# Performance work log

Measured on AMD Instinct MI355X. Metric: run time of the kernel, lower is better.

The kernel has to match this reference:

```python
import jax, jax.numpy as jnp
import numpy as np

EMB = 512
HEADS = 8
HD = EMB // HEADS
DEPTH = 6
CONT = 100
CAT_DIMS = [100] * 28
CAT = len(CAT_DIMS)
HID = int(EMB * (4.0 / 3.0))  # 682, FT-Transformer ReGLU hidden
B = 128
OFFSETS = jnp.asarray(np.concatenate([[0], np.cumsum(CAT_DIMS[:-1])]).astype(np.int32))
SQRT_EMB = float(np.sqrt(EMB))  # scores are DIVIDED by emb**-0.5 in the source


def setup_inputs() -> dict:
    key = jax.random.key(0)
    ks = jax.random.split(key, 16)
    s = 0.02
    x_cat = jax.random.randint(ks[0], (B, CAT), 0, CAT_DIMS[0]).astype(jnp.float32)
    x_cont = jax.random.normal(ks[1], (B, CONT), dtype=jnp.float32)
    x = jnp.concatenate([x_cat, x_cont], axis=1)  # [B, CAT+CONT]
    return {
        "x": x,
        "tok_w": jax.random.normal(ks[2], (CONT + 1, EMB)) * s,
        "tok_b": jax.random.normal(ks[3], (CONT + CAT, EMB)) * s,
        "cat_emb": jax.random.normal(ks[4], (sum(CAT_DIMS), EMB)) * s,
        "Wqkv": jax.random.normal(ks[5], (DEPTH, EMB, 3 * EMB)) * s,
        "bqkv": jnp.zeros((DEPTH, 3 * EMB)),
        "Wout": jax.random.normal(ks[6], (DEPTH, EMB, EMB)) * s,
        "bout": jnp.zeros((DEPTH, EMB)),
        "W0": jax.random.normal(ks[7], (DEPTH, EMB, 2 * HID)) * s,
        "b0": jnp.zeros((DEPTH, 2 * HID)),
        "W1": jax.random.normal(ks[8], (DEPTH, HID, EMB)) * s,
        "b1": jnp.zeros((DEPTH, EMB)),
        "ln0_g": jnp.ones((DEPTH, EMB)),
        "ln0_b": jnp.zeros((DEPTH, EMB)),
        "ln1_g": jnp.ones((DEPTH, EMB)),
        "ln1_b": jnp.zeros((DEPTH, EMB)),
    }


def _ln(x, g, b):
    m = x.mean(-1, keepdims=True)
    v = x.var(-1, keepdims=True)
    return (x - m) / jnp.sqrt(v + 1e-5) * g + b


def _attn(x, Wqkv, bqkv, Wout, bout):
    Bn, S, _ = x.shape
    # faithful layout: reshape to (B,S,H,3*hd), move heads, chunk last dim
    qkv = (x @ Wqkv + bqkv).reshape(Bn, S, HEADS, 3 * HD).transpose(0, 2, 1, 3)
    q, k, v = jnp.split(qkv, 3, axis=-1)  # each [B,H,S,hd]
    scores = jnp.einsum("bhqd,bhkd->bhqk", q, k) * SQRT_EMB  # / (emb**-0.5)
    attn = jax.nn.softmax(jax.nn.softmax(scores, axis=-1), axis=-1)  # double softmax, as in source
    o = jnp.einsum("bhqk,bhkd->bhqd", attn, v)
    o = o.transpose(0, 2, 1, 3).reshape(Bn, S, EMB)
    return o @ Wout + bout


def _reglu(x):
    a, b = jnp.split(x, 2, axis=-1)
    return a * jax.nn.relu(b)


def _forward(x, tok_w, tok_b, cat_emb, Wqkv, bqkv, Wout, bout, W0, b0, W1, b1,
             ln0_g, ln0_b, ln1_g, ln1_b):
    # --- feature tokenizer ---
    x_cats = x[:, :CAT].astype(jnp.int32)
    x_conts = jnp.concatenate([jnp.ones((x.shape[0], 1), x.dtype), x[:, CAT:]], axis=1)  # [B, CONT+1]
    h = tok_w[None] * x_conts[:, :, None]  # [B, CONT+1, EMB]
    h = jnp.concatenate([h, cat_emb[x_cats + OFFSETS[None]]], axis=1)  # [B, S=129, EMB]
    bias = jnp.concatenate([jnp.zeros((1, EMB), h.dtype), tok_b], axis=0)
    h = h + bias[None]
    # --- transformer stack ---
    for i in range(DEPTH):
        xin = _ln(h, ln0_g[i], ln0_b[i]) if i else h  # layer 0 has no norm0
        h = h + _attn(xin, Wqkv[i], bqkv[i], Wout[i], bout[i])
        r = _ln(h, ln1_g[i], ln1_b[i])
        r = _reglu(r @ W0[i] + b0[i]) @ W1[i] + b1[i]
        h = h + r
    return h[:, 0]  # CLS token


def reference(x, tok_w, tok_b, cat_emb, Wqkv, bqkv, Wout, bout, W0, b0, W1, b1,
              ln0_g, ln0_b, ln1_g, ln1_b):
    return _forward(x, tok_w, tok_b, cat_emb, Wqkv, bqkv, Wout, bout, W0, b0, W1, b1,
                    ln0_g, ln0_b, ln1_g, ln1_b)
```

## Files before the change

kernel.cpp:

```cpp
#include <hip/hip_runtime.h>
#include <hip/hip_bf16.h>
#include <stdint.h>


typedef __hip_bfloat16 bf16_t;
typedef __attribute__((ext_vector_type(8))) __bf16 bf16x8;
typedef __attribute__((ext_vector_type(4))) float floatx4;

constexpr int M_ROWS = 16512;
constexpr float SQRT_EMB_F = 22.627416997969522f;

__device__ __forceinline__ floatx4 mfma16(bf16x8 a, bf16x8 b, floatx4 c) {
  return __builtin_amdgcn_mfma_f32_16x16x32_bf16(a, b, c, 0, 0, 0);
}

__device__ __forceinline__ size_t frag_chunk(int m, int k, int KT) {
  return ((size_t)(m >> 4) * KT + (k >> 5)) * 512 + (m & 15) * 8 + 128 * ((k >> 3) & 3);
}
__device__ __forceinline__ size_t frag_elem(int m, int k, int KT) {
  return frag_chunk(m, k, KT) + (k & 7);
}

template <int PERM>
__global__ __launch_bounds__(256) void transpose_cvt(const float* __restrict__ W,
    bf16_t* __restrict__ WT, int K, int N, int KP, int NP)
{
  __shared__ float tile[32][33];
  int k0 = blockIdx.x * 32, n0 = blockIdx.y * 32;
  const float* Wl = W + (size_t)blockIdx.z * K * N;
  bf16_t* WTl = WT + (size_t)blockIdx.z * NP * KP;
  const int KT = KP >> 5;
  #pragma unroll
  for (int r = 0; r < 32; r += 8) {
    int k = k0 + threadIdx.y + r, n = n0 + threadIdx.x;
    int srcn = PERM ? ((n & 1) ? 682 + (n >> 1) : (n >> 1)) : n;
    int valid = (k < K) && (PERM ? (n < 1364) : (n < N));
    tile[threadIdx.y + r][threadIdx.x] = valid ? Wl[(size_t)k * N + srcn] : 0.f;
  }
  __syncthreads();
  #pragma unroll
  for (int r = 0; r < 32; r += 8) {
    int n = n0 + threadIdx.y + r, k = k0 + threadIdx.x;
    if (n < NP && k < KP)
      WTl[frag_elem(n, k, KT)] = __float2bfloat16(tile[threadIdx.x][threadIdx.y + r]);
  }
}

__global__ __launch_bounds__(256) void tokenizer_kernel(const float* __restrict__ x,
    const float* __restrict__ tok_w, const float* __restrict__ tok_b,
    const float* __restrict__ cat_emb, float* __restrict__ h, bf16_t* __restrict__ ab)
{
  int row = blockIdx.x * 4 + (threadIdx.x >> 6);
  int lane = threadIdx.x & 63, e0 = lane * 8;
  int b = row / 129, t = row - b * 129;
  float v[8];
  if (t == 0) {
    #pragma unroll
    for (int u = 0; u < 8; u++) v[u] = tok_w[e0 + u];
  } else if (t <= 100) {
    float xv = x[(size_t)b * 128 + 28 + (t - 1)];
    const float* wp = tok_w + (size_t)t * 512 + e0;
    const float* bp = tok_b + (size_t)(t - 1) * 512 + e0;
    #pragma unroll
    for (int u = 0; u < 8; u++) v[u] = wp[u] * xv + bp[u];
  } else {
    int j = t - 101;
    int idx = (int)x[(size_t)b * 128 + j] + 100 * j;
    const float* cp = cat_emb + (size_t)idx * 512 + e0;
    const float* bp = tok_b + (size_t)(t - 1) * 512 + e0;
    #pragma unroll
    for (int u = 0; u < 8; u++) v[u] = cp[u] + bp[u];
  }
  float* hr = h + (size_t)row * 512 + e0;
  #pragma unroll
  for (int u = 0; u < 8; u++) hr[u] = v[u];
  bf16x8 o8;
  #pragma unroll
  for (int u = 0; u < 8; u++) o8[u] = (__bf16)__float2bfloat16(v[u]);
  *(bf16x8*)(ab + ((size_t)(row >> 4) * 16 + (lane >> 2)) * 512 + (row & 15) * 8 + 128 * (lane & 3)) = o8;
}

__global__ __launch_bounds__(256) void ln_kernel(const float* __restrict__ hin,
    bf16_t* __restrict__ out, const float* __restrict__ g, const float* __restrict__ bta)
{
  int row = blockIdx.x * 4 + (threadIdx.x >> 6);
  int lane = threadIdx.x & 63;
  const float* hr = hin + (size_t)row * 512 + lane * 8;
  float4 v0 = *(const float4*)hr;
  float4 v1 = *(const float4*)(hr + 4);
  float s = v0.x + v0.y + v0.z + v0.w + v1.x + v1.y + v1.z + v1.w;
  float q = v0.x * v0.x + v0.y * v0.y + v0.z * v0.z + v0.w * v0.w
          + v1.x * v1.x + v1.y * v1.y + v1.z * v1.z + v1.w * v1.w;
  #pragma unroll
  for (int o = 1; o < 64; o <<= 1) { s += __shfl_xor(s, o); q += __shfl_xor(q, o); }
  float mean = s * (1.f / 512.f);
  float var = q * (1.f / 512.f) - mean * mean;
  float rstd = rsqrtf(var + 1e-5f);
  float4 g0 = *(const float4*)(g + lane * 8);
  float4 g1 = *(const float4*)(g + lane * 8 + 4);
  float4 b0v = *(const float4*)(bta + lane * 8);
  float4 b1v = *(const float4*)(bta + lane * 8 + 4);
  bf16x8 o8;
  o8[0] = (__bf16)__float2bfloat16((v0.x - mean) * rstd * g0.x + b0v.x);
  o8[1] = (__bf16)__float2bfloat16((v0.y - mean) * rstd * g0.y + b0v.y);
  o8[2] = (__bf16)__float2bfloat16((v0.z - mean) * rstd * g0.z + b0v.z);
  o8[3] = (__bf16)__float2bfloat16((v0.w - mean) * rstd * g0.w + b0v.w);
  o8[4] = (__bf16)__float2bfloat16((v1.x - mean) * rstd * g1.x + b1v.x);
  o8[5] = (__bf16)__float2bfloat16((v1.y - mean) * rstd * g1.y + b1v.y);
  o8[6] = (__bf16)__float2bfloat16((v1.z - mean) * rstd * g1.z + b1v.z);
  o8[7] = (__bf16)__float2bfloat16((v1.w - mean) * rstd * g1.w + b1v.w);
  *(bf16x8*)(out + ((size_t)(row >> 4) * 16 + (lane >> 2)) * 512 + (row & 15) * 8 + 128 * (lane & 3)) = o8;
}

template <int MODE>
__global__ __launch_bounds__(256, 3) void gemm_frag(const bf16_t* __restrict__ A,
    const bf16_t* __restrict__ BT, const float* __restrict__ bias, int biasN,
    const float* __restrict__ resid, void* __restrict__ outp, int K, int N)
{
  const int total = gridDim.x * gridDim.y;
  const int lin = blockIdx.y * gridDim.x + blockIdx.x;
  const int xcd = lin & 7, kb2 = lin >> 3;
  const int qch = total >> 3, rch = total & 7;
  const int idx = xcd * qch + (xcd < rch ? xcd : rch) + kb2;
  const int bm = idx / gridDim.x;
  const int bn = idx - bm * gridDim.x;
  const int m0 = bm * 128, n0 = bn * 128;

  const int tid = threadIdx.x;
  const int w = tid >> 6, l = tid & 63, l15 = l & 15, quad = l >> 4;
  const int wm = (w >> 1) * 64, wn = (w & 1) * 64;
  const int KT = K >> 5;

  const bf16_t* pa[4];
  const bf16_t* pb[4];
  #pragma unroll
  for (int i = 0; i < 4; i++) {
    pa[i] = A  + ((size_t)(((m0 + wm) >> 4) + i) * KT) * 512 + l * 8;
    pb[i] = BT + ((size_t)(((n0 + wn) >> 4) + i) * KT) * 512 + l * 8;
  }

  bf16x8 af[2][4], bg[2][4];
  #pragma unroll
  for (int i = 0; i < 4; i++) {
    af[0][i] = *(const bf16x8*)pa[i];
    bg[0][i] = *(const bf16x8*)pb[i];
  }

  floatx4 z4 = {0.f, 0.f, 0.f, 0.f};
  floatx4 acc[4][4];
  #pragma unroll
  for (int i = 0; i < 4; i++)
    #pragma unroll
    for (int j = 0; j < 4; j++) acc[i][j] = z4;

  const int T = KT;
  for (int t = 0; t < T; t += 2) {
    if (t + 1 < T) {
      #pragma unroll
      for (int i = 0; i < 4; i++) {
        af[1][i] = *(const bf16x8*)(pa[i] + (size_t)(t + 1) * 512);
        bg[1][i] = *(const bf16x8*)(pb[i] + (size_t)(t + 1) * 512);
      }
    }
    #pragma unroll
    for (int i = 0; i < 4; i++)
      #pragma unroll
      for (int j = 0; j < 4; j++)
        acc[i][j] = mfma16(af[0][i], bg[0][j], acc[i][j]);
    if (t + 1 < T) {
      if (t + 2 < T) {
        #pragma unroll
        for (int i = 0; i < 4; i++) {
          af[0][i] = *(const bf16x8*)(pa[i] + (size_t)(t + 2) * 512);
          bg[0][i] = *(const bf16x8*)(pb[i] + (size_t)(t + 2) * 512);
        }
      }
      #pragma unroll
      for (int i = 0; i < 4; i++)
        #pragma unroll
        for (int j = 0; j < 4; j++)
          acc[i][j] = mfma16(af[1][i], bg[1][j], acc[i][j]);
    }
  }

  #pragma unroll
  for (int j = 0; j < 4; j++) {
    int col = n0 + wn + j * 16 + l15;
    float bv = 0.f;
    if (MODE == 2) {
      if (col < biasN) bv = bias[(col & 1) ? 682 + (col >> 1) : (col >> 1)];
    } else {
      if (col < biasN) bv = bias[col];
    }
    #pragma unroll
    for (int i = 0; i < 4; i++) {
      int row_b = m0 + wm + i * 16 + quad * 4;
      #pragma unroll
      for (int r = 0; r < 4; r++) {
        float v = acc[i][j][r] + bv;
        int m = row_b + r;
        if (MODE == 2) {
          float other = __shfl_xor(v, 1);
          if (!(l15 & 1)) {
            int c2 = col >> 1;
            ((bf16_t*)outp)[frag_elem(m, c2, (N >> 1) >> 5)] =
                __float2bfloat16(v * fmaxf(other, 0.f));
          }
        } else if (MODE == 1) {
          size_t idx2 = (size_t)m * N + col;
          ((float*)outp)[idx2] = v + resid[idx2];
        } else {
          ((bf16_t*)outp)[frag_elem(m, col, N >> 5)] = __float2bfloat16(v);
        }
      }
    }
  }
}

constexpr int SP = 160;
__global__ __launch_bounds__(256) void attn_kernel(const bf16_t* __restrict__ qkv,
                                                   bf16_t* __restrict__ attnout)
{
  __shared__ bf16_t vt_lds[64 * SP];
  __shared__ float sc[32 * SP];
  bf16_t* p_lds = (bf16_t*)sc;
  __bf16* vt_raw = (__bf16*)vt_lds;

  const int bh = blockIdx.x, b = bh >> 3, hh = bh & 7;
  const int tid = threadIdx.x;
  const int w = tid >> 6, l = tid & 63, l15 = l & 15, quad = l >> 4;
  const int rbase = b * 129;

  for (int i = tid; i < SP * 64 / 2; i += 256) ((unsigned int*)vt_lds)[i] = 0u;
  __syncthreads();
  for (int c = tid; c < 129 * 8; c += 256) {
    int s = c >> 3, ch = c & 7;
    bf16x8 tv = *(const bf16x8*)(qkv + frag_chunk(rbase + s, hh * 192 + 128 + ch * 8, 48));
    #pragma unroll
    for (int j = 0; j < 8; j++) vt_raw[(size_t)(ch * 8 + j) * SP + s] = tv[j];
  }
  __syncthreads();

  for (int qt = 0; qt < 5; qt++) {
    bf16x8 zq = {};
    bf16x8 aq[2][2];
    #pragma unroll
    for (int mt = 0; mt < 2; mt++) {
      int m = qt * 32 + mt * 16 + l15;
      #pragma unroll
      for (int t = 0; t < 2; t++)
        aq[mt][t] = (m < 129)
            ? *(const bf16x8*)(qkv + frag_chunk(rbase + m, hh * 192 + t * 32 + quad * 8, 48)) : zq;
    }
    for (int nt = w; nt < 10; nt += 4) {
      int krow = nt * 16 + l15;
      floatx4 a0 = {0.f, 0.f, 0.f, 0.f}, a1 = {0.f, 0.f, 0.f, 0.f};
      #pragma unroll
      for (int t = 0; t < 2; t++) {
        bf16x8 kf = (krow < 129)
            ? *(const bf16x8*)(qkv + frag_chunk(rbase + krow, hh * 192 + 64 + t * 32 + quad * 8, 48))
            : zq;
        a0 = mfma16(aq[0][t], kf, a0);
        a1 = mfma16(aq[1][t], kf, a1);
      }
      #pragma unroll
      for (int r = 0; r < 4; r++) {
        sc[(quad * 4 + r) * SP + nt * 16 + l15]      = a0[r] * SQRT_EMB_F;
        sc[(16 + quad * 4 + r) * SP + nt * 16 + l15] = a1[r] * SQRT_EMB_F;
      }
    }
    __syncthreads();

    {
      int row = tid >> 3, sub = tid & 7;
      float vv[20];
      float mx = -1e30f;
      #pragma unroll
      for (int c = 0; c < 20; c++) {
        int j = sub + c * 8;
        vv[c] = (j < 129) ? sc[row * SP + j] : -1e30f;
        mx = fmaxf(mx, vv[c]);
      }
      #pragma unroll
      for (int o = 1; o < 8; o <<= 1) mx = fmaxf(mx, __shfl_xor(mx, o, 8));
      float sum = 0.f;
      #pragma unroll
      for (int c = 0; c < 20; c++) {
        int j = sub + c * 8;
        vv[c] = (j < 129) ? __expf(vv[c] - mx) : 0.f;
        sum += vv[c];
      }
      #pragma unroll
      for (int o = 1; o < 8; o <<= 1) sum += __shfl_xor(sum, o, 8);
      float inv = 1.f / sum;
      float mx2 = 0.f;
      #pragma unroll
      for (int c = 0; c < 20; c++) { vv[c] *= inv; mx2 = fmaxf(mx2, vv[c]); }
      #pragma unroll
      for (int o = 1; o < 8; o <<= 1) mx2 = fmaxf(mx2, __shfl_xor(mx2, o, 8));
      float sum2 = 0.f;
      #pragma unroll
      for (int c = 0; c < 20; c++) {
        int j = sub + c * 8;
        vv[c] = (j < 129) ? __expf(vv[c] - mx2) : 0.f;
        sum2 += vv[c];
      }
      #pragma unroll
      for (int o = 1; o < 8; o <<= 1) sum2 += __shfl_xor(sum2, o, 8);
      float inv2 = 1.f / sum2;
      __syncthreads();
      #pragma unroll
      for (int c = 0; c < 20; c++) {
        int j = sub + c * 8;
        p_lds[row * SP + j] = __float2bfloat16(vv[c] * inv2);
      }
    }
    __syncthreads();

    {
      int mt = w >> 1, nt0 = (w & 1) * 2;
      floatx4 oacc[2];
      oacc[0] = floatx4{0.f, 0.f, 0.f, 0.f};
      oacc[1] = floatx4{0.f, 0.f, 0.f, 0.f};
      #pragma unroll
      for (int t = 0; t < 5; t++) {
        bf16x8 pf = *(const bf16x8*)&p_lds[(mt * 16 + l15) * SP + t * 32 + quad * 8];
        #pragma unroll
        for (int n = 0; n < 2; n++) {
          bf16x8 vf = *(const bf16x8*)&vt_lds[((nt0 + n) * 16 + l15) * SP + t * 32 + quad * 8];
          oacc[n] = mfma16(pf, vf, oacc[n]);
        }
      }
      #pragma unroll
      for (int n = 0; n < 2; n++)
        #pragma unroll
        for (int r = 0; r < 4; r++) {
          int sq = qt * 32 + mt * 16 + quad * 4 + r;
          if (sq < 129) {
            int cc = hh * 64 + (nt0 + n) * 16 + l15;
            attnout[frag_elem(rbase + sq, cc, 16)] = __float2bfloat16(oacc[n][r]);
          }
        }
    }
    __syncthreads();
  }
}

__global__ __launch_bounds__(256) void out_copy(const float* __restrict__ h,
                                                float* __restrict__ out)
{
  int b = blockIdx.x, e = threadIdx.x;
  out[(size_t)b * 512 + e]       = h[(size_t)b * 129 * 512 + e];
  out[(size_t)b * 512 + e + 256] = h[(size_t)b * 129 * 512 + e + 256];
}

extern "C" void kernel_launch(void* const* d_in, const int* in_sizes, int n_in,
                              void* d_out, int out_size, void* d_ws, size_t ws_size,
                              hipStream_t stream)
{
  const float* x       = (const float*)d_in[0];
  const float* tok_w   = (const float*)d_in[1];
  const float* tok_b   = (const float*)d_in[2];
  const float* cat_emb = (const float*)d_in[3];
  const float* Wqkv    = (const float*)d_in[4];
  const float* bqkv    = (const float*)d_in[5];
  const float* Wout    = (const float*)d_in[6];
  const float* bout    = (const float*)d_in[7];
  const float* W0      = (const float*)d_in[8];
  const float* b0      = (const float*)d_in[9];
  const float* W1      = (const float*)d_in[10];
  const float* b1      = (const float*)d_in[11];
  const float* ln0_g   = (const float*)d_in[12];
  const float* ln0_b   = (const float*)d_in[13];
  const float* ln1_g   = (const float*)d_in[14];
  const float* ln1_b   = (const float*)d_in[15];

  size_t off = 0;
  char* base = (char*)d_ws;
  auto alloc = [&](size_t n) { char* p = base + off; off += (n + 255) & ~(size_t)255; return p; };
  float*  h     = (float*) alloc((size_t)M_ROWS * 512 * 4);
  bf16_t* ab    = (bf16_t*)alloc((size_t)M_ROWS * 512 * 2);
  bf16_t* qkv   = (bf16_t*)alloc((size_t)M_ROWS * 1536 * 2);
  bf16_t* attno = (bf16_t*)alloc((size_t)M_ROWS * 512 * 2);
  bf16_t* regl  = (bf16_t*)alloc((size_t)M_ROWS * 704 * 2);
  bf16_t* WqkvT = (bf16_t*)alloc((size_t)6 * 1536 * 512 * 2);
  bf16_t* WoutT = (bf16_t*)alloc((size_t)6 * 512 * 512 * 2);
  bf16_t* W0T   = (bf16_t*)alloc((size_t)6 * 1408 * 512 * 2);
  bf16_t* W1T   = (bf16_t*)alloc((size_t)6 * 512 * 704 * 2);
  (void)ws_size; (void)in_sizes; (void)n_in; (void)out_size;

  dim3 tb(32, 8, 1);
  transpose_cvt<0><<<dim3(16, 48, 6), tb, 0, stream>>>(Wqkv, WqkvT, 512, 1536, 512, 1536);
  transpose_cvt<0><<<dim3(16, 16, 6), tb, 0, stream>>>(Wout, WoutT, 512, 512, 512, 512);
  transpose_cvt<1><<<dim3(16, 44, 6), tb, 0, stream>>>(W0, W0T, 512, 1364, 512, 1408);
  transpose_cvt<0><<<dim3(22, 16, 6), tb, 0, stream>>>(W1, W1T, 682, 512, 704, 512);

  tokenizer_kernel<<<M_ROWS / 4, 256, 0, stream>>>(x, tok_w, tok_b, cat_emb, h, ab);

  for (int i = 0; i < 6; i++) {
    if (i)
      ln_kernel<<<M_ROWS / 4, 256, 0, stream>>>(h, ab, ln0_g + (size_t)i * 512,
                                                ln0_b + (size_t)i * 512);
    gemm_frag<0><<<dim3(12, 129), 256, 0, stream>>>(
        ab, WqkvT + (size_t)i * 1536 * 512, bqkv + (size_t)i * 1536, 1536, nullptr, qkv, 512, 1536);
    attn_kernel<<<1024, 256, 0, stream>>>(qkv, attno);
    gemm_frag<1><<<dim3(4, 129), 256, 0, stream>>>(
        attno, WoutT + (size_t)i * 512 * 512, bout + (size_t)i * 512, 512, h, h, 512, 512);
    ln_kernel<<<M_ROWS / 4, 256, 0, stream>>>(h, ab, ln1_g + (size_t)i * 512,
                                              ln1_b + (size_t)i * 512);
    gemm_frag<2><<<dim3(11, 129), 256, 0, stream>>>(
        ab, W0T + (size_t)i * 1408 * 512, b0 + (size_t)i * 1364, 1364, nullptr, regl, 512, 1408);
    gemm_frag<1><<<dim3(4, 129), 256, 0, stream>>>(
        regl, W1T + (size_t)i * 512 * 704, b1 + (size_t)i * 512, 512, h, h, 704, 512);
  }

  out_copy<<<128, 256, 0, stream>>>(h, (float*)d_out);
}
```

Before: 1.273 ms.

## Give each wave one query tile and keep attention scores in registers

The attention kernel now runs 5 waves (320 threads), each owning one 32-row query tile, instead of 4 waves looping over 5 query tiles with block-wide barriers. Scores stay in MFMA accumulator registers and the double softmax is reduced with 16-lane shuffles, so the fp32 score round trip through LDS and most __syncthreads are gone. Each wave writes its own private P buffer and runs the full PV product itself. The cost is higher register pressure (the 18 score accumulators plus the output tiles) and more LDS for the five P buffers, which could lower occupancy.

```diff
diff --git a/kernel.cpp b/kernel.cpp
--- a/kernel.cpp
+++ b/kernel.cpp
@@ -217,133 +217,139 @@
   }
 }
 
-constexpr int SP = 160;
-__global__ __launch_bounds__(256) void attn_kernel(const bf16_t* __restrict__ qkv,
+constexpr int SPP = 168;
+__global__ __launch_bounds__(320) void attn_kernel(const bf16_t* __restrict__ qkv,
                                                    bf16_t* __restrict__ attnout)
 {
-  __shared__ bf16_t vt_lds[64 * SP];
-  __shared__ float sc[32 * SP];
-  bf16_t* p_lds = (bf16_t*)sc;
-  __bf16* vt_raw = (__bf16*)vt_lds;
+  __shared__ __align__(16) __bf16 vt_lds[64 * SPP];
+  __shared__ __align__(16) __bf16 p_lds[5][32 * SPP];
 
   const int bh = blockIdx.x, b = bh >> 3, hh = bh & 7;
   const int tid = threadIdx.x;
-  const int w = tid >> 6, l = tid & 63, l15 = l & 15, quad = l >> 4;
+  const int w = tid / 64, l = tid & 63, l15 = l & 15, quad = l >> 4;
   const int rbase = b * 129;
 
-  for (int i = tid; i < SP * 64 / 2; i += 256) ((unsigned int*)vt_lds)[i] = 0u;
+  for (int i = tid; i < 64 * SPP / 2; i += 320) ((unsigned int*)vt_lds)[i] = 0u;
   __syncthreads();
-  for (int c = tid; c < 129 * 8; c += 256) {
+  for (int c = tid; c < 129 * 8; c += 320) {
     int s = c >> 3, ch = c & 7;
     bf16x8 tv = *(const bf16x8*)(qkv + frag_chunk(rbase + s, hh * 192 + 128 + ch * 8, 48));
     #pragma unroll
-    for (int j = 0; j < 8; j++) vt_raw[(size_t)(ch * 8 + j) * SP + s] = tv[j];
+    for (int j = 0; j < 8; j++) vt_lds[(size_t)(ch * 8 + j) * SPP + s] = tv[j];
   }
   __syncthreads();
 
-  for (int qt = 0; qt < 5; qt++) {
-    bf16x8 zq = {};
-    bf16x8 aq[2][2];
-    #pragma unroll
-    for (int mt = 0; mt < 2; mt++) {
-      int m = qt * 32 + mt * 16 + l15;
-      #pragma unroll
-      for (int t = 0; t < 2; t++)
-        aq[mt][t] = (m < 129)
-            ? *(const bf16x8*)(qkv + frag_chunk(rbase + m, hh * 192 + t * 32 + quad * 8, 48)) : zq;
-    }
-    for (int nt = w; nt < 10; nt += 4) {
-      int krow = nt * 16 + l15;
-      floatx4 a0 = {0.f, 0.f, 0.f, 0.f}, a1 = {0.f, 0.f, 0.f, 0.f};
-      #pragma unroll
-      for (int t = 0; t < 2; t++) {
-        bf16x8 kf = (krow < 129)
-            ? *(const bf16x8*)(qkv + frag_chunk(rbase + krow, hh * 192 + 64 + t * 32 + quad * 8, 48))
-            : zq;
-        a0 = mfma16(aq[0][t], kf, a0);
-        a1 = mfma16(aq[1][t], kf, a1);
-      }
-      #pragma unroll
-      for (int r = 0; r < 4; r++) {
-        sc[(quad * 4 + r) * SP + nt * 16 + l15]      = a0[r] * SQRT_EMB_F;
-        sc[(16 + quad * 4 + r) * SP + nt * 16 + l15] = a1[r] * SQRT_EMB_F;
-      }
-    }
-    __syncthreads();
-
-    {
-      int row = tid >> 3, sub = tid & 7;
-      float vv[20];
+  const int qt = w;
+  __bf16* pw = p_lds[w];
+
+  bf16x8 zq = {};
+  bf16x8 aq[2][2];
+  #pragma unroll
+  for (int mt = 0; mt < 2; mt++) {
+    int m = qt * 32 + mt * 16 + l15;
+    #pragma unroll
+    for (int t = 0; t < 2; t++)
+      aq[mt][t] = (m < 129)
+          ? *(const bf16x8*)(qkv + frag_chunk(rbase + m, hh * 192 + t * 32 + quad * 8, 48)) : zq;
+  }
+
+  floatx4 z4 = {0.f, 0.f, 0.f, 0.f};
+  floatx4 sc[2][9];
+  #pragma unroll
+  for (int mt = 0; mt < 2; mt++)
+    #pragma unroll
+    for (int nt = 0; nt < 9; nt++) sc[mt][nt] = z4;
+  #pragma unroll
+  for (int nt = 0; nt < 9; nt++) {
+    int krow = nt * 16 + l15;
+    #pragma unroll
+    for (int t = 0; t < 2; t++) {
+      bf16x8 kf = (krow < 129)
+          ? *(const bf16x8*)(qkv + frag_chunk(rbase + krow, hh * 192 + 64 + t * 32 + quad * 8, 48))
+          : zq;
+      sc[0][nt] = mfma16(aq[0][t], kf, sc[0][nt]);
+      sc[1][nt] = mfma16(aq[1][t], kf, sc[1][nt]);
+    }
+  }
+
+  const bool v8 = (l15 == 0);
+  #pragma unroll
+  for (int mt = 0; mt < 2; mt++) {
+    #pragma unroll
+    for (int r = 0; r < 4; r++) {
+      float v[9];
+      #pragma unroll
+      for (int nt = 0; nt < 9; nt++) v[nt] = sc[mt][nt][r] * SQRT_EMB_F;
       float mx = -1e30f;
       #pragma unroll
-      for (int c = 0; c < 20; c++) {
-        int j = sub + c * 8;
-        vv[c] = (j < 129) ? sc[row * SP + j] : -1e30f;
-        mx = fmaxf(mx, vv[c]);
-      }
-      #pragma unroll
-      for (int o = 1; o < 8; o <<= 1) mx = fmaxf(mx, __shfl_xor(mx, o, 8));
+      for (int nt = 0; nt < 8; nt++) mx = fmaxf(mx, v[nt]);
+      if (v8) mx = fmaxf(mx, v[8]);
+      #pragma unroll
+      for (int o = 1; o < 16; o <<= 1) mx = fmaxf(mx, __shfl_xor(mx, o));
       float sum = 0.f;
       #pragma unroll
-      for (int c = 0; c < 20; c++) {
-        int j = sub + c * 8;
-        vv[c] = (j < 129) ? __expf(vv[c] - mx) : 0.f;
-        sum += vv[c];
-      }
-      #pragma unroll
-      for (int o = 1; o < 8; o <<= 1) sum += __shfl_xor(sum, o, 8);
+      for (int nt = 0; nt < 8; nt++) { v[nt] = __expf(v[nt] - mx); sum += v[nt]; }
+      v[8] = v8 ? __expf(v[8] - mx) : 0.f;
+      sum += v[8];
+      #pragma unroll
+      for (int o = 1; o < 16; o <<= 1) sum += __shfl_xor(sum, o);
       float inv = 1.f / sum;
       float mx2 = 0.f;
       #pragma unroll
-      for (int c = 0; c < 20; c++) { vv[c] *= inv; mx2 = fmaxf(mx2, vv[c]); }
-      #pragma unroll
-      for (int o = 1; o < 8; o <<= 1) mx2 = fmaxf(mx2, __shfl_xor(mx2, o, 8));
+      for (int nt = 0; nt < 9; nt++) { v[nt] *= inv; mx2 = fmaxf(mx2, v[nt]); }
+      #pragma unroll
+      for (int o = 1; o < 16; o <<= 1) mx2 = fmaxf(mx2, __shfl_xor(mx2, o));
       float sum2 = 0.f;
       #pragma unroll
-      for (int c = 0; c < 20; c++) {
-        int j = sub + c * 8;
-        vv[c] = (j < 129) ? __expf(vv[c] - mx2) : 0.f;
-        sum2 += vv[c];
+      for (int nt = 0; nt < 8; nt++) { v[nt] = __expf(v[nt] - mx2); sum2 += v[nt]; }
+      v[8] = v8 ? __expf(v[8] - mx2) : 0.f;
+      sum2 += v[8];
+      #pragma unroll
+      for (int o = 1; o < 16; o <<= 1) sum2 += __shfl_xor(sum2, o);
+      float inv2 = 1.f / sum2;
+      int row = mt * 16 + quad * 4 + r;
+      #pragma unroll
+      for (int nt = 0; nt < 9; nt++) {
+        float pv = (nt < 8 || v8) ? v[nt] * inv2 : 0.f;
+        pw[(size_t)row * SPP + nt * 16 + l15] = __bf16(__float2bfloat16(pv));
       }
-      #pragma unroll
-      for (int o = 1; o < 8; o <<= 1) sum2 += __shfl_xor(sum2, o, 8);
-      float inv2 = 1.f / sum2;
-      __syncthreads();
-      #pragma unroll
-      for (int c = 0; c < 20; c++) {
-        int j = sub + c * 8;
-        p_lds[row * SP + j] = __float2bfloat16(vv[c] * inv2);
-      }
-    }
-    __syncthreads();
-
-    {
-      int mt = w >> 1, nt0 = (w & 1) * 2;
-      floatx4 oacc[2];
-      oacc[0] = floatx4{0.f, 0.f, 0.f, 0.f};
-      oacc[1] = floatx4{0.f, 0.f, 0.f, 0.f};
-      #pragma unroll
-      for (int t = 0; t < 5; t++) {
-        bf16x8 pf = *(const bf16x8*)&p_lds[(mt * 16 + l15) * SP + t * 32 + quad * 8];
-        #pragma unroll
-        for (int n = 0; n < 2; n++) {
-          bf16x8 vf = *(const bf16x8*)&vt_lds[((nt0 + n) * 16 + l15) * SP + t * 32 + quad * 8];
-          oacc[n] = mfma16(pf, vf, oacc[n]);
+      pw[(size_t)row * SPP + 144 + l15] = __bf16(0.0f);
+    }
+  }
+  asm volatile("" ::: "memory");
+
+  floatx4 oacc[2][4];
+  #pragma unroll
+  for (int mt = 0; mt < 2; mt++)
+    #pragma unroll
+    for (int dt = 0; dt < 4; dt++) oacc[mt][dt] = z4;
+  #pragma unroll
+  for (int kt = 0; kt < 5; kt++) {
+    bf16x8 pf[2], vf[4];
+    #pragma unroll
+    for (int mt = 0; mt < 2; mt++)
+      pf[mt] = *(const bf16x8*)&pw[(size_t)(mt * 16 + l15) * SPP + kt * 32 + quad * 8];
+    #pragma unroll
+    for (int dt = 0; dt < 4; dt++)
+      vf[dt] = *(const bf16x8*)&vt_lds[(size_t)(dt * 16 + l15) * SPP + kt * 32 + quad * 8];
+    #pragma unroll
+    for (int mt = 0; mt < 2; mt++)
+      #pragma unroll
+      for (int dt = 0; dt < 4; dt++)
+        oacc[mt][dt] = mfma16(pf[mt], vf[dt], oacc[mt][dt]);
+  }
+  #pragma unroll
+  for (int mt = 0; mt < 2; mt++)
+    #pragma unroll
+    for (int dt = 0; dt < 4; dt++)
+      #pragma unroll
+      for (int r = 0; r < 4; r++) {
+        int sq = qt * 32 + mt * 16 + quad * 4 + r;
+        if (sq < 129) {
+          int cc = hh * 64 + dt * 16 + l15;
+          attnout[frag_elem(rbase + sq, cc, 16)] = __float2bfloat16(oacc[mt][dt][r]);
         }
       }
-      #pragma unroll
-      for (int n = 0; n < 2; n++)
-        #pragma unroll
-        for (int r = 0; r < 4; r++) {
-          int sq = qt * 32 + mt * 16 + quad * 4 + r;
-          if (sq < 129) {
-            int cc = hh * 64 + (nt0 + n) * 16 + l15;
-            attnout[frag_elem(rbase + sq, cc, 16)] = __float2bfloat16(oacc[n][r]);
-          }
-        }
-    }
-    __syncthreads();
-  }
 }
 
 __global__ __launch_bounds__(256) void out_copy(const float* __restrict__ h,
@@ -403,7 +409,7 @@
                                                 ln0_b + (size_t)i * 512);
     gemm_frag<0><<<dim3(12, 129), 256, 0, stream>>>(
         ab, WqkvT + (size_t)i * 1536 * 512, bqkv + (size_t)i * 1536, 1536, nullptr, qkv, 512, 1536);
-    attn_kernel<<<1024, 256, 0, stream>>>(qkv, attno);
+    attn_kernel<<<1024, 320, 0, stream>>>(qkv, attno);
     gemm_frag<1><<<dim3(4, 129), 256, 0, stream>>>(
         attno, WoutT + (size_t)i * 512 * 512, bout + (size_t)i * 512, 512, h, h, 512, 512);
     ln_kernel<<<M_ROWS / 4, 256, 0, stream>>>(h, ab, ln1_g + (size_t)i * 512,
```

Result: slower. 1.358 ms (+6.6%).
